# Kernel tuning notes

Measured on AMD Instinct MI355X. Metric: run time of the kernel, lower is better.

The kernel has to match this reference:

```python
import jax, jax.numpy as jnp
import numpy as np

B, U1, U2 = 4, 2048, 2048
C = 256      # in_feat_dim
F = 256      # feat_dim
M = 4        # num_modes
D = C // M   # attention_mode_dim = 64
ATTN_CLIP = 500.0
LN_EPS = 1e-12


def setup_inputs() -> dict:
    key = jax.random.key(0)
    ks = jax.random.split(key, 8)
    s = 0.02  # base_initializer_range
    inp = {
        "query_feat": jax.random.normal(ks[0], (B, U1, C), jnp.float32),
        "key_feat": jax.random.normal(ks[1], (B, U2, C), jnp.float32),
        "Wq": jax.random.normal(ks[2], (M * D, C), jnp.float32) * s,
        "bq": jnp.zeros((M * D,), jnp.float32),
    }
    # tie_qk_scheme='shared': key linear shares query weights
    inp["Wk"] = inp["Wq"]
    inp["bk"] = inp["bq"]
    inp["Wv"] = jax.random.normal(ks[3], (M * F, C), jnp.float32) * s  # first_linear, v_has_bias=False
    inp["W_mid"] = jax.random.normal(ks[4], (F, F), jnp.float32) * s   # MMSharedMid shared_linear
    inp["b_mid"] = jnp.zeros((F,), jnp.float32)
    inp["W_out"] = jax.random.normal(ks[5], (M, F, F), jnp.float32) * s  # grouped 1x1 conv, per mode
    inp["b_out"] = jnp.zeros((M, F), jnp.float32)
    inp["ln_g"] = jnp.ones((F,), jnp.float32)   # resout LayerNorm
    inp["ln_b"] = jnp.zeros((F,), jnp.float32)
    inp["W_score"] = jax.random.normal(ks[6], (1, F), jnp.float32) * s  # LearnedSoftAggregate
    inp["b_score"] = jnp.zeros((1,), jnp.float32)
    return inp


def _layer_norm(x, g, b):
    mu = jnp.mean(x, axis=-1, keepdims=True)
    var = jnp.var(x, axis=-1, keepdims=True)
    return (x - mu) * jax.lax.rsqrt(var + LN_EPS) * g + b


def reference(query_feat, key_feat, Wq, bq, Wk, bk, Wv, W_mid, b_mid,
              W_out, b_out, ln_g, ln_b, W_score, b_score):
    # --- tied-QK multi-mode attention ---
    q = (query_feat @ Wq.T + bq).reshape(B, U1, M, D)
    k = (key_feat @ Wk.T + bk).reshape(B, U2, M, D)
    scores = jnp.einsum('bimd,bjmd->bmij', q, k) / jnp.sqrt(jnp.float32(D))
    scores = jnp.clip(scores, -ATTN_CLIP, ATTN_CLIP)  # attn_clip
    probs = jax.nn.softmax(scores, axis=-1)           # [B, M, U1, U2]

    # --- ExpandedFeatTrans: value projection + fusion ---
    v = (key_feat @ Wv.T).reshape(B, U2, M, F)        # first_linear (no bias)
    fused = jnp.einsum('bmij,bjmf->bmif', probs, v)   # [B, M, U1, F]

    # MMSharedMid: shared linear over F + gelu (dropout = identity in eval)
    mid = jax.nn.gelu(fused @ W_mid.T + b_mid, approximate=False)

    # MMPrivateOutput: per-mode grouped 1x1 conv; NOTE the original code computes
    # x_comb = x + shortcut but then layer-norms x (shortcut dropped) - kept faithful.
    out = jnp.einsum('bmif,mgf->bmig', mid, W_out) + b_out[None, :, None, :]
    out = _layer_norm(out, ln_g, ln_b)                # [B, M, U1, F]

    # LearnedSoftAggregate over modes (group_dim=1, keepdim=False)
    mode_scores = out @ W_score.T + b_score           # [B, M, U1, 1]
    mode_probs = jax.nn.softmax(mode_scores, axis=1)
    return jnp.sum(out * mode_probs, axis=1)          # [B, U1, F]
```

## Files before the change

kernel.cpp:

```cpp
#include <hip/hip_runtime.h>

typedef __attribute__((ext_vector_type(8))) short short8;
typedef __attribute__((ext_vector_type(4))) float f32x4;
typedef __attribute__((ext_vector_type(16))) float f32x16;
typedef unsigned short u16t;
typedef unsigned int u32t;

#define MFMA16(a, b, c) __builtin_amdgcn_mfma_f32_16x16x32_bf16((a), (b), (c), 0, 0, 0)
#define MFMA32(a, b, c) __builtin_amdgcn_mfma_f32_32x32x16_bf16((a), (b), (c), 0, 0, 0)

__device__ __forceinline__ u16t f2bf(float f) {
  u32t u = __float_as_uint(f);
  u32t r = u + 0x7fffu + ((u >> 16) & 1u);
  return (u16t)(r >> 16);
}
__device__ __forceinline__ float bf2f(u16t b) {
  return __uint_as_float(((u32t)b) << 16);
}
__device__ __forceinline__ short8 pack8(float4 a0, float4 a1) {
  short8 r;
  r[0] = (short)f2bf(a0.x); r[1] = (short)f2bf(a0.y);
  r[2] = (short)f2bf(a0.z); r[3] = (short)f2bf(a0.w);
  r[4] = (short)f2bf(a1.x); r[5] = (short)f2bf(a1.y);
  r[6] = (short)f2bf(a1.z); r[7] = (short)f2bf(a1.w);
  return r;
}
__device__ __forceinline__ u32t packrhu(float a, float b) {
  u32t ua = __float_as_uint(a) + 0x8000u;
  u32t ub = __float_as_uint(b) + 0x8000u;
  return (ua >> 16) | (ub & 0xffff0000u);
}

__global__ void cvt_kernel(const float* __restrict__ src, u16t* __restrict__ dst, int n) {
  int i = blockIdx.x * 256 + threadIdx.x;
  if (i < n) dst[i] = f2bf(src[i]);
}

__global__ __launch_bounds__(256) void proj_gemm(
    const float* __restrict__ A, const float* __restrict__ W,
    const float* __restrict__ bias,
    u16t* __restrict__ out, int mode) {
  __shared__ __align__(16) u16t As[64 * 72];
  __shared__ __align__(16) u16t Ws[64 * 72];
  const int tid = threadIdx.x;
  const int w = tid >> 6, lane = tid & 63, quad = lane >> 4, l15 = lane & 15;
  const int l31 = lane & 31, h8 = (lane >> 5) * 8;
  const int rt = blockIdx.x * 64;
  const int ct = blockIdx.y * 64;
  const int wrow = (w >> 1) * 32, wcol = (w & 1) * 32;
  const int r2 = tid >> 3, c8 = tid & 7;

  const f32x4 fzero = {0.f, 0.f, 0.f, 0.f};
  f32x4 acc[2][2];
#pragma unroll
  for (int i = 0; i < 2; i++)
#pragma unroll
    for (int j = 0; j < 2; j++) acc[i][j] = fzero;

  for (int kt = 0; kt < 4; ++kt) {
    __syncthreads();
#pragma unroll
    for (int hh = 0; hh < 2; ++hh) {
      int rr = r2 + hh * 32;
      const float4* pa = (const float4*)(A + (size_t)(rt + rr) * 256 + kt * 64 + c8 * 8);
      const float4* pw = (const float4*)(W + (size_t)(ct + rr) * 256 + kt * 64 + c8 * 8);
      *(short8*)&As[rr * 72 + c8 * 8] = pack8(pa[0], pa[1]);
      *(short8*)&Ws[rr * 72 + c8 * 8] = pack8(pw[0], pw[1]);
    }
    __syncthreads();
#pragma unroll
    for (int ks = 0; ks < 2; ++ks) {
      short8 af0 = *(const short8*)&As[(wrow + l15) * 72 + ks * 32 + quad * 8];
      short8 af1 = *(const short8*)&As[(wrow + 16 + l15) * 72 + ks * 32 + quad * 8];
      short8 bw0 = *(const short8*)&Ws[(wcol + l15) * 72 + ks * 32 + quad * 8];
      short8 bw1 = *(const short8*)&Ws[(wcol + 16 + l15) * 72 + ks * 32 + quad * 8];
      acc[0][0] = MFMA16(af0, bw0, acc[0][0]);
      acc[0][1] = MFMA16(af0, bw1, acc[0][1]);
      acc[1][0] = MFMA16(af1, bw0, acc[1][0]);
      acc[1][1] = MFMA16(af1, bw1, acc[1][1]);
    }
  }

  __syncthreads();
  u16t* Cs = As;
  if (mode == 0) {
#pragma unroll
    for (int i = 0; i < 2; i++) {
      int rl = wrow + i * 16 + quad * 4;
#pragma unroll
      for (int j = 0; j < 2; j++) {
        int cl = wcol + j * 16 + l15;
        float bv = bias ? bias[ct + cl] : 0.f;
#pragma unroll
        for (int rg = 0; rg < 4; ++rg)
          Cs[(rl + rg) * 72 + cl] = f2bf(acc[i][j][rg] + bv);
      }
    }
  } else {
#pragma unroll
    for (int i = 0; i < 2; i++) {
      int rl = wrow + i * 16 + quad * 4;
#pragma unroll
      for (int j = 0; j < 2; j++) {
        int cl = wcol + j * 16 + l15;
        ushort4 pk;
        pk.x = f2bf(acc[i][j][0]);
        pk.y = f2bf(acc[i][j][1]);
        pk.z = f2bf(acc[i][j][2]);
        pk.w = f2bf(acc[i][j][3]);
        *(ushort4*)&Cs[cl * 72 + rl] = pk;
      }
    }
  }
  __syncthreads();

#pragma unroll
  for (int t2 = 0; t2 < 2; ++t2) {
    short8 frag = *(const short8*)&Cs[(t2 * 32 + l31) * 72 + w * 16 + h8];
    size_t base;
    if (mode == 0) {
      int b = rt >> 11, m = blockIdx.y;
      int it32 = ((rt & 2047) >> 5) + t2;
      base = (((size_t)(b * 4 + m) * 64 + it32) * 4 + w) * 512;
    } else {
      int b = rt >> 11, m = blockIdx.y >> 2;
      int fb = ((blockIdx.y & 3) << 1) + t2;
      int jt16 = ((rt & 2047) >> 4) + w;
      base = (((size_t)(b * 4 + m) * 8 + fb) * 128 + jt16) * 512;
    }
    *(short8*)(out + base + lane * 8) = frag;
  }
}

__global__ __launch_bounds__(256, 3) void attn_kernel(
    const u16t* __restrict__ Qf, const u16t* __restrict__ Kf,
    const u16t* __restrict__ Vf,
    const u16t* __restrict__ Wmid, const u16t* __restrict__ Wout,
    const float* __restrict__ b_mid, const float* __restrict__ b_out,
    const float* __restrict__ ln_g, const float* __restrict__ ln_b,
    const float* __restrict__ Wsc, const float* __restrict__ b_sc,
    u16t* __restrict__ out_ln, float* __restrict__ scoresWS) {
  __shared__ __align__(16) u16t smF[32 * 264];
  __shared__ __align__(16) u16t smP[2][32 * 132];
  __shared__ float smL[128];
  __shared__ float smR[128];
  __shared__ float smS[64];
  const int tid = threadIdx.x;
  const int w = tid >> 6, lane = tid & 63, quad = lane >> 4, l15 = lane & 15;
  const int l31 = lane & 31, h = lane >> 5;
  const int it32 = blockIdx.x;
  const int bm = blockIdx.y, m = bm & 3;
  const int q0 = it32 * 32;

  const size_t lane8 = (size_t)lane * 8;

  const u16t* qbase = Qf + ((size_t)(bm * 64 + it32) * 4) * 512 + lane8;
  short8 qf4[4];
#pragma unroll
  for (int ksd = 0; ksd < 4; ++ksd)
    qf4[ksd] = *(const short8*)(qbase + ksd * 512);

  const u16t* kbase = Kf + ((size_t)bm * 256) * 512 + lane8;
  const u16t* vbase = Vf + ((size_t)(bm * 8 + 2 * w) * 128) * 512 + lane8;

  f32x16 facc[2];
#pragma unroll
  for (int j = 0; j < 2; j++)
#pragma unroll
    for (int r = 0; r < 16; r++) facc[j][r] = 0.f;
  float lsum = 0.f;

#pragma unroll 1
  for (int t = 0; t < 16; ++t) {
    u16t* Pb = &smP[t & 1][0];
    const int jt32 = t * 4 + w;
    short8 kf4[4];
#pragma unroll
    for (int ksd = 0; ksd < 4; ++ksd)
      kf4[ksd] = *(const short8*)(kbase + (size_t)jt32 * 2048 + ksd * 512);

    f32x16 sacc;
#pragma unroll
    for (int r = 0; r < 16; r++) sacc[r] = 0.f;
#pragma unroll
    for (int ksd = 0; ksd < 4; ++ksd)
      sacc = MFMA32(kf4[ksd], qf4[ksd], sacc);

    float ls = 0.f;
#pragma unroll
    for (int tt = 0; tt < 8; ++tt) {
      float p0 = __expf(sacc[2 * tt] * 0.125f);
      float p1 = __expf(sacc[2 * tt + 1] * 0.125f);
      ls += p0 + p1;
      const int jl = ((2 * tt) & 3) + 8 * ((2 * tt) >> 2) + 4 * h;
      *(u32t*)&Pb[l31 * 132 + w * 32 + jl] = packrhu(p0, p1);
    }
    lsum += ls;

    __syncthreads();

#pragma unroll
    for (int jj = 0; jj < 4; ++jj) {
      short8 vf[2][2];
#pragma unroll
      for (int fb = 0; fb < 2; ++fb)
#pragma unroll
        for (int ks2 = 0; ks2 < 2; ++ks2)
          vf[fb][ks2] = *(const short8*)(vbase + ((size_t)fb * 128 + (t * 8 + jj * 2 + ks2)) * 512);
      short8 bbL[2];
#pragma unroll
      for (int ks2 = 0; ks2 < 2; ++ks2)
        bbL[ks2] = *(const short8*)&Pb[l31 * 132 + jj * 32 + ks2 * 16 + h * 8];
      facc[0] = MFMA32(vf[0][0], bbL[0], facc[0]);
      facc[0] = MFMA32(vf[0][1], bbL[1], facc[0]);
      facc[1] = MFMA32(vf[1][0], bbL[0], facc[1]);
      facc[1] = MFMA32(vf[1][1], bbL[1], facc[1]);
    }
  }

  lsum += __shfl_xor(lsum, 32);
  if (h == 0) smL[w * 32 + l31] = lsum;
  __syncthreads();
  float inv = 1.f / (smL[l31] + smL[32 + l31] + smL[64 + l31] + smL[96 + l31]);

#pragma unroll
  for (int fb = 0; fb < 2; ++fb) {
#pragma unroll
    for (int g = 0; g < 4; ++g) {
      int fbase = w * 64 + fb * 32 + 8 * g + 4 * h;
      ushort4 pk4;
      pk4.x = f2bf(facc[fb][4 * g + 0] * inv);
      pk4.y = f2bf(facc[fb][4 * g + 1] * inv);
      pk4.z = f2bf(facc[fb][4 * g + 2] * inv);
      pk4.w = f2bf(facc[fb][4 * g + 3] * inv);
      *(ushort4*)&smF[l31 * 264 + fbase] = pk4;
    }
  }
  __syncthreads();

  const int rgrp = w >> 1, ch = w & 1;
  const int rowq = rgrp * 16 + quad * 4;
  const f32x4 fz4 = {0.f, 0.f, 0.f, 0.f};

  f32x4 macc[8];
#pragma unroll
  for (int i = 0; i < 8; i++) macc[i] = fz4;
  for (int kc = 0; kc < 8; ++kc) {
    short8 af = *(const short8*)&smF[(rgrp * 16 + l15) * 264 + kc * 32 + quad * 8];
#pragma unroll
    for (int nb = 0; nb < 8; ++nb) {
      short8 bw = *(const short8*)(Wmid + (size_t)(ch * 128 + nb * 16 + l15) * 256 + kc * 32 + quad * 8);
      macc[nb] = MFMA16(af, bw, macc[nb]);
    }
  }
#pragma unroll
  for (int nb = 0; nb < 8; ++nb) {
    int c = ch * 128 + nb * 16 + l15;
    float bmv = b_mid[c];
#pragma unroll
    for (int rg = 0; rg < 4; ++rg) {
      float x = macc[nb][rg] + bmv;
      macc[nb][rg] = 0.5f * x * (1.f + erff(x * 0.70710678118654752f));
    }
  }
  __syncthreads();
#pragma unroll
  for (int nb = 0; nb < 8; ++nb)
#pragma unroll
    for (int rg = 0; rg < 4; ++rg)
      smF[(rowq + rg) * 264 + ch * 128 + nb * 16 + l15] = f2bf(macc[nb][rg]);
  __syncthreads();

  const u16t* Wo = Wout + (size_t)m * 65536;
  f32x4 oacc[8];
#pragma unroll
  for (int i = 0; i < 8; i++) oacc[i] = fz4;
  for (int kc = 0; kc < 8; ++kc) {
    short8 af = *(const short8*)&smF[(rgrp * 16 + l15) * 264 + kc * 32 + quad * 8];
#pragma unroll
    for (int nb = 0; nb < 8; ++nb) {
      short8 bw = *(const short8*)(Wo + (size_t)(ch * 128 + nb * 16 + l15) * 256 + kc * 32 + quad * 8);
      oacc[nb] = MFMA16(af, bw, oacc[nb]);
    }
  }

  float sum[4] = {0, 0, 0, 0}, sq[4] = {0, 0, 0, 0};
#pragma unroll
  for (int nb = 0; nb < 8; ++nb) {
    int c = ch * 128 + nb * 16 + l15;
    float bo = b_out[m * 256 + c];
#pragma unroll
    for (int rg = 0; rg < 4; ++rg) {
      float x = oacc[nb][rg] + bo;
      oacc[nb][rg] = x;
      sum[rg] += x;
      sq[rg] += x * x;
    }
  }
#pragma unroll
  for (int rg = 0; rg < 4; ++rg) {
    float s = sum[rg], s2 = sq[rg];
    s += __shfl_xor(s, 1); s += __shfl_xor(s, 2); s += __shfl_xor(s, 4); s += __shfl_xor(s, 8);
    s2 += __shfl_xor(s2, 1); s2 += __shfl_xor(s2, 2); s2 += __shfl_xor(s2, 4); s2 += __shfl_xor(s2, 8);
    if (l15 == 0) {
      smR[(rowq + rg) + 32 * ch] = s;
      smR[64 + (rowq + rg) + 32 * ch] = s2;
    }
  }
  __syncthreads();
  float mu[4], rstd[4];
#pragma unroll
  for (int rg = 0; rg < 4; ++rg) {
    int r = rowq + rg;
    float s = smR[r] + smR[r + 32];
    float s2 = smR[64 + r] + smR[64 + r + 32];
    float mean = s * (1.f / 256.f);
    float var = s2 * (1.f / 256.f) - mean * mean;
    mu[rg] = mean;
    rstd[rg] = rsqrtf(var + 1e-12f);
  }

  float scp[4] = {0, 0, 0, 0};
#pragma unroll
  for (int nb = 0; nb < 8; ++nb) {
    int c = ch * 128 + nb * 16 + l15;
    float g = ln_g[c], bb2 = ln_b[c], wsv = Wsc[c];
#pragma unroll
    for (int rg = 0; rg < 4; ++rg) {
      float xn = (oacc[nb][rg] - mu[rg]) * rstd[rg] * g + bb2;
      out_ln[((size_t)bm * 2048 + (q0 + rowq + rg)) * 256 + c] = f2bf(xn);
      scp[rg] += xn * wsv;
    }
  }
#pragma unroll
  for (int rg = 0; rg < 4; ++rg) {
    float s = scp[rg];
    s += __shfl_xor(s, 1); s += __shfl_xor(s, 2); s += __shfl_xor(s, 4); s += __shfl_xor(s, 8);
    if (l15 == 0) smS[(rowq + rg) + 32 * ch] = s;
  }
  __syncthreads();
  if (ch == 0 && l15 == 0) {
#pragma unroll
    for (int rg = 0; rg < 4; ++rg) {
      int r = rowq + rg;
      scoresWS[bm * 2048 + q0 + r] = smS[r] + smS[r + 32] + b_sc[0];
    }
  }
}

__global__ __launch_bounds__(256) void agg_kernel(
    const u16t* __restrict__ out_ln, const float* __restrict__ scoresWS,
    float* __restrict__ out) {
  const int row = blockIdx.x;
  const int c = threadIdx.x;
  const int b = row >> 11, i = row & 2047;
  float s0 = scoresWS[(b * 4 + 0) * 2048 + i];
  float s1 = scoresWS[(b * 4 + 1) * 2048 + i];
  float s2 = scoresWS[(b * 4 + 2) * 2048 + i];
  float s3 = scoresWS[(b * 4 + 3) * 2048 + i];
  float mx = fmaxf(fmaxf(s0, s1), fmaxf(s2, s3));
  float e0 = __expf(s0 - mx), e1 = __expf(s1 - mx), e2 = __expf(s2 - mx), e3 = __expf(s3 - mx);
  float inv = 1.f / (e0 + e1 + e2 + e3);
  float acc = e0 * inv * bf2f(out_ln[((size_t)(b * 4 + 0) * 2048 + i) * 256 + c]) +
              e1 * inv * bf2f(out_ln[((size_t)(b * 4 + 1) * 2048 + i) * 256 + c]) +
              e2 * inv * bf2f(out_ln[((size_t)(b * 4 + 2) * 2048 + i) * 256 + c]) +
              e3 * inv * bf2f(out_ln[((size_t)(b * 4 + 3) * 2048 + i) * 256 + c]);
  out[(size_t)row * 256 + c] = acc;
}

extern "C" void kernel_launch(void* const* d_in, const int* in_sizes, int n_in,
                              void* d_out, int out_size, void* d_ws, size_t ws_size,
                              hipStream_t stream) {
  (void)in_sizes; (void)n_in; (void)out_size; (void)ws_size;
  const float* query = (const float*)d_in[0];
  const float* key   = (const float*)d_in[1];
  const float* Wq    = (const float*)d_in[2];
  const float* bq    = (const float*)d_in[3];
  const float* Wv    = (const float*)d_in[6];
  const float* Wm    = (const float*)d_in[7];
  const float* bmid  = (const float*)d_in[8];
  const float* Wo    = (const float*)d_in[9];
  const float* bo    = (const float*)d_in[10];
  const float* lng   = (const float*)d_in[11];
  const float* lnb   = (const float*)d_in[12];
  const float* Wsc   = (const float*)d_in[13];
  const float* bsc   = (const float*)d_in[14];

  char* p = (char*)d_ws;
  u16t* QfB = (u16t*)p; p += (size_t)2097152 * 2;
  u16t* KfB = (u16t*)p; p += (size_t)2097152 * 2;
  u16t* VfB = (u16t*)p; p += (size_t)8388608 * 2;
  u16t* WmB = (u16t*)p; p += (size_t)65536 * 2;
  u16t* WoB = (u16t*)p; p += (size_t)262144 * 2;
  u16t* outLn = (u16t*)p; p += (size_t)8388608 * 2;
  float* scWS = (float*)p; p += (size_t)32768 * 4;

  cvt_kernel<<<256, 256, 0, stream>>>(Wm, WmB, 65536);
  cvt_kernel<<<1024, 256, 0, stream>>>(Wo, WoB, 262144);

  proj_gemm<<<dim3(128, 4), 256, 0, stream>>>(query, Wq, bq, QfB, 0);
  proj_gemm<<<dim3(128, 4), 256, 0, stream>>>(key, Wq, bq, KfB, 0);
  proj_gemm<<<dim3(128, 16), 256, 0, stream>>>(key, Wv, nullptr, VfB, 1);

  attn_kernel<<<dim3(64, 16), 256, 0, stream>>>(QfB, KfB, VfB, WmB, WoB,
                                                bmid, bo, lng, lnb, Wsc, bsc,
                                                outLn, scWS);

  agg_kernel<<<8192, 256, 0, stream>>>(outLn, scWS, (float*)d_out);
}
```

Baseline: 252.1 us.

## Prefetch next K tile, fold softmax scale into Q projection, remap blocks per XCD

The attention kernel now loads the next iteration's K fragments right after the barrier, so the load overlaps the P·V MFMAs instead of stalling at the top of the loop. The 1/sqrt(D) scale moves into the Q projection weights and bias, which drops one multiply per score in the exp loop. Block indices are remapped so each XCD handles two contiguous batch-mode slices, which should give better L2 reuse of K and V. The prefetch adds register pressure under launch_bounds(256,3), and scaling before bf16 rounding changes numerics slightly.

After: 255.2 us. Within noise of the previous version (+1.2%).

```diff
diff --git a/kernel.cpp b/kernel.cpp
--- a/kernel.cpp
+++ b/kernel.cpp
@@ -38,7 +38,7 @@
 
 __global__ __launch_bounds__(256) void proj_gemm(
     const float* __restrict__ A, const float* __restrict__ W,
-    const float* __restrict__ bias,
+    const float* __restrict__ bias, float scale,
     u16t* __restrict__ out, int mode) {
   __shared__ __align__(16) u16t As[64 * 72];
   __shared__ __align__(16) u16t Ws[64 * 72];
@@ -64,8 +64,11 @@
       int rr = r2 + hh * 32;
       const float4* pa = (const float4*)(A + (size_t)(rt + rr) * 256 + kt * 64 + c8 * 8);
       const float4* pw = (const float4*)(W + (size_t)(ct + rr) * 256 + kt * 64 + c8 * 8);
+      float4 w0 = pw[0], w1 = pw[1];
+      w0.x *= scale; w0.y *= scale; w0.z *= scale; w0.w *= scale;
+      w1.x *= scale; w1.y *= scale; w1.z *= scale; w1.w *= scale;
       *(short8*)&As[rr * 72 + c8 * 8] = pack8(pa[0], pa[1]);
-      *(short8*)&Ws[rr * 72 + c8 * 8] = pack8(pw[0], pw[1]);
+      *(short8*)&Ws[rr * 72 + c8 * 8] = pack8(w0, w1);
     }
     __syncthreads();
 #pragma unroll
@@ -90,7 +93,7 @@
 #pragma unroll
       for (int j = 0; j < 2; j++) {
         int cl = wcol + j * 16 + l15;
-        float bv = bias ? bias[ct + cl] : 0.f;
+        float bv = bias ? bias[ct + cl] * scale : 0.f;
 #pragma unroll
         for (int rg = 0; rg < 4; ++rg)
           Cs[(rl + rg) * 72 + cl] = f2bf(acc[i][j][rg] + bv);
@@ -148,8 +151,11 @@
   const int tid = threadIdx.x;
   const int w = tid >> 6, lane = tid & 63, quad = lane >> 4, l15 = lane & 15;
   const int l31 = lane & 31, h = lane >> 5;
-  const int it32 = blockIdx.x;
-  const int bm = blockIdx.y, m = bm & 3;
+  const int L = blockIdx.y * 64 + blockIdx.x;
+  const int xcd = L & 7, slot = L >> 3;
+  const int bm = xcd * 2 + (slot >> 6);
+  const int it32 = slot & 63;
+  const int m = bm & 3;
   const int q0 = it32 * 32;
 
   const size_t lane8 = (size_t)lane * 8;
@@ -169,16 +175,15 @@
 #pragma unroll
     for (int r = 0; r < 16; r++) facc[j][r] = 0.f;
   float lsum = 0.f;
+
+  short8 kf4[4];
+#pragma unroll
+  for (int ksd = 0; ksd < 4; ++ksd)
+    kf4[ksd] = *(const short8*)(kbase + (size_t)w * 2048 + ksd * 512);
 
 #pragma unroll 1
   for (int t = 0; t < 16; ++t) {
     u16t* Pb = &smP[t & 1][0];
-    const int jt32 = t * 4 + w;
-    short8 kf4[4];
-#pragma unroll
-    for (int ksd = 0; ksd < 4; ++ksd)
-      kf4[ksd] = *(const short8*)(kbase + (size_t)jt32 * 2048 + ksd * 512);
-
     f32x16 sacc;
 #pragma unroll
     for (int r = 0; r < 16; r++) sacc[r] = 0.f;
@@ -189,8 +194,8 @@
     float ls = 0.f;
 #pragma unroll
     for (int tt = 0; tt < 8; ++tt) {
-      float p0 = __expf(sacc[2 * tt] * 0.125f);
-      float p1 = __expf(sacc[2 * tt + 1] * 0.125f);
+      float p0 = __expf(sacc[2 * tt]);
+      float p1 = __expf(sacc[2 * tt + 1]);
       ls += p0 + p1;
       const int jl = ((2 * tt) & 3) + 8 * ((2 * tt) >> 2) + 4 * h;
       *(u32t*)&Pb[l31 * 132 + w * 32 + jl] = packrhu(p0, p1);
@@ -199,6 +204,12 @@
 
     __syncthreads();
 
+    if (t < 15) {
+      const int jt32n = (t + 1) * 4 + w;
+#pragma unroll
+      for (int ksd = 0; ksd < 4; ++ksd)
+        kf4[ksd] = *(const short8*)(kbase + (size_t)jt32n * 2048 + ksd * 512);
+    }
 #pragma unroll
     for (int jj = 0; jj < 4; ++jj) {
       short8 vf[2][2];
@@ -398,9 +409,9 @@
   cvt_kernel<<<256, 256, 0, stream>>>(Wm, WmB, 65536);
   cvt_kernel<<<1024, 256, 0, stream>>>(Wo, WoB, 262144);
 
-  proj_gemm<<<dim3(128, 4), 256, 0, stream>>>(query, Wq, bq, QfB, 0);
-  proj_gemm<<<dim3(128, 4), 256, 0, stream>>>(key, Wq, bq, KfB, 0);
-  proj_gemm<<<dim3(128, 16), 256, 0, stream>>>(key, Wv, nullptr, VfB, 1);
+  proj_gemm<<<dim3(128, 4), 256, 0, stream>>>(query, Wq, bq, 0.125f, QfB, 0);
+  proj_gemm<<<dim3(128, 4), 256, 0, stream>>>(key, Wq, bq, 1.0f, KfB, 0);
+  proj_gemm<<<dim3(128, 16), 256, 0, stream>>>(key, Wv, nullptr, 1.0f, VfB, 1);
 
   attn_kernel<<<dim3(64, 16), 256, 0, stream>>>(QfB, KfB, VfB, WmB, WoB,
                                                 bmid, bo, lng, lnb, Wsc, bsc,
```
